# Kernel tuning notes

Measured on AMD Instinct MI355X. Metric: run time of the kernel, lower is better.

Reference implementation:

```python
import jax, jax.numpy as jnp
import numpy as np

BN_EPS = 1e-5

def conv1x1(x, w, b):
    # x: [B,C,H,W], w: [O,C], b: [O]
    return jnp.einsum('bchw,oc->bohw', x, w) + b[None, :, None, None]

def bn_inf(x, gamma, beta, mean, var):
    inv = gamma / jnp.sqrt(var + BN_EPS)
    return (x - mean[None, :, None, None]) * inv[None, :, None, None] + beta[None, :, None, None]

def setup_inputs() -> dict:
    key = jax.random.key(0)
    ks = jax.random.split(key, 24)
    B, Fg, Fl, Fi = 8, 256, 256, 64
    H = W = 64
    c8 = Fi // 8
    d = {}
    d['g'] = jax.random.normal(ks[0], (B, Fg, H, W), jnp.float32)
    d['x'] = jax.random.normal(ks[1], (B, Fl, H, W), jnp.float32)
    # W_g: conv1x1 + BN
    d['Wg_w'] = jax.random.normal(ks[2], (Fi, Fg), jnp.float32) * (1.0 / np.sqrt(Fg))
    d['Wg_b'] = jax.random.normal(ks[3], (Fi,), jnp.float32) * 0.02
    d['bng_gamma'] = jax.random.uniform(ks[4], (Fi,), jnp.float32, 0.5, 1.5)
    d['bng_beta'] = jax.random.normal(ks[5], (Fi,), jnp.float32) * 0.1
    d['bng_mean'] = jax.random.normal(ks[6], (Fi,), jnp.float32) * 0.1
    d['bng_var'] = jax.random.uniform(ks[7], (Fi,), jnp.float32, 0.5, 1.5)
    # W_x: conv1x1 + BN
    d['Wx_w'] = jax.random.normal(ks[8], (Fi, Fl), jnp.float32) * (1.0 / np.sqrt(Fl))
    d['Wx_b'] = jax.random.normal(ks[9], (Fi,), jnp.float32) * 0.02
    d['bnx_gamma'] = jax.random.uniform(ks[10], (Fi,), jnp.float32, 0.5, 1.5)
    d['bnx_beta'] = jax.random.normal(ks[11], (Fi,), jnp.float32) * 0.1
    d['bnx_mean'] = jax.random.normal(ks[12], (Fi,), jnp.float32) * 0.1
    d['bnx_var'] = jax.random.uniform(ks[13], (Fi,), jnp.float32, 0.5, 1.5)
    # psi: conv1x1 (Fi->1) + BN(1) + sigmoid
    d['psi_w'] = jax.random.normal(ks[14], (1, Fi), jnp.float32) * (1.0 / np.sqrt(Fi))
    d['psi_b'] = jax.random.normal(ks[15], (1,), jnp.float32) * 0.02
    d['bnp_gamma'] = jax.random.uniform(ks[16], (1,), jnp.float32, 0.5, 1.5)
    d['bnp_beta'] = jax.random.normal(ks[17], (1,), jnp.float32) * 0.1
    d['bnp_mean'] = jax.random.normal(ks[18], (1,), jnp.float32) * 0.1
    d['bnp_var'] = jax.random.uniform(ks[19], (1,), jnp.float32, 0.5, 1.5)
    # PAM convs
    d['pb_w'] = jax.random.normal(ks[20], (c8, Fi), jnp.float32) * (1.0 / np.sqrt(Fi))
    d['pb_b'] = jnp.zeros((c8,), jnp.float32)
    d['pc_w'] = jax.random.normal(ks[21], (c8, Fi), jnp.float32) * (1.0 / np.sqrt(Fi))
    d['pc_b'] = jnp.zeros((c8,), jnp.float32)
    d['pd_w'] = jax.random.normal(ks[22], (Fi, Fi), jnp.float32) * (1.0 / np.sqrt(Fi))
    d['pd_b'] = jnp.zeros((Fi,), jnp.float32)
    # scalar gates (torch inits to 0; use small nonzero to exercise the path)
    d['alpha'] = jax.random.normal(ks[23], (1,), jnp.float32) * 0.05
    d['cam_beta'] = jax.random.normal(jax.random.fold_in(key, 99), (1,), jnp.float32) * 0.05
    return d

def _cam(psi, cam_beta):
    B, C, H, W = psi.shape
    feat = psi.reshape(B, C, H * W)                       # [B,C,HW]
    att = jnp.einsum('bcn,bdn->bcd', feat, feat)          # [B,C,C]
    att_new = jnp.max(att, axis=-1, keepdims=True) - att  # max-subtract trick
    att = jax.nn.softmax(att_new, axis=-1)
    out = jnp.einsum('bcd,bdn->bcn', att, feat).reshape(B, C, H, W)
    return cam_beta[0] * out + psi

def _pam(psi, pb_w, pb_b, pc_w, pc_b, pd_w, pd_b, alpha):
    B, C, H, W = psi.shape
    HW = H * W
    fb = conv1x1(psi, pb_w, pb_b).reshape(B, -1, HW)      # [B,C/8,HW]
    fc = conv1x1(psi, pc_w, pc_b).reshape(B, -1, HW)      # [B,C/8,HW]
    energy = jnp.einsum('bki,bkj->bij', fb, fc)           # [B,HW,HW]
    att = jax.nn.softmax(energy, axis=-1)
    fd = conv1x1(psi, pd_w, pd_b).reshape(B, C, HW)       # [B,C,HW]
    out = jnp.einsum('bcj,bij->bci', fd, att).reshape(B, C, H, W)
    return alpha[0] * out + psi

def reference(g, x, Wg_w, Wg_b, bng_gamma, bng_beta, bng_mean, bng_var,
              Wx_w, Wx_b, bnx_gamma, bnx_beta, bnx_mean, bnx_var,
              psi_w, psi_b, bnp_gamma, bnp_beta, bnp_mean, bnp_var,
              pb_w, pb_b, pc_w, pc_b, pd_w, pd_b, alpha, cam_beta):
    g1 = bn_inf(conv1x1(g, Wg_w, Wg_b), bng_gamma, bng_beta, bng_mean, bng_var)
    x1 = bn_inf(conv1x1(x, Wx_w, Wx_b), bnx_gamma, bnx_beta, bnx_mean, bnx_var)
    psi = jax.nn.relu(g1 + x1)                            # [B,F_int,H,W]
    cam = _cam(psi, cam_beta)
    pam = _pam(psi, pb_w, pb_b, pc_w, pc_b, pd_w, pd_b, alpha)
    gate = bn_inf(conv1x1(cam * pam, psi_w, psi_b), bnp_gamma, bnp_beta, bnp_mean, bnp_var)
    da = jax.nn.sigmoid(gate)                             # [B,1,H,W]
    return x * da
```

## Files before the change

### kernel.cpp

```cpp
#include <hip/hip_runtime.h>
#include <hip/hip_bf16.h>
#include <math.h>

#define BB 8
#define CIN 256
#define FI 64
#define HW 4096
#define C8 8
#define EPS 1e-5f
#define LOG2E 1.4426950408889634f

typedef __attribute__((ext_vector_type(8))) short bf16x8;
typedef __attribute__((ext_vector_type(4))) float f32x4;
typedef __attribute__((ext_vector_type(4))) unsigned u32x4;
typedef unsigned short u16;

static __device__ __forceinline__ u16 f2b(float x) {
    unsigned u = __builtin_bit_cast(unsigned, x);
    return (u16)((u + 0x8000u) >> 16);
}
static __device__ __forceinline__ unsigned pk2(float a, float b) {
    unsigned ua = __builtin_bit_cast(unsigned, a);
    unsigned ub = __builtin_bit_cast(unsigned, b);
    return ((ua + 0x8000u) >> 16) | ((ub + 0x8000u) & 0xffff0000u);
}
static __device__ __forceinline__ unsigned cvtpk(float a, float b) {
    unsigned r;
    asm("v_cvt_pk_bf16_f32 %0, %1, %2" : "=v"(r) : "v"(a), "v"(b));
    return r;
}
static __device__ __forceinline__ float b2f(u16 v) {
    return __builtin_bit_cast(float, ((unsigned)v) << 16);
}

__global__ __launch_bounds__(256) void k_prep(
    const float* __restrict__ Wg, const float* __restrict__ Wgb,
    const float* __restrict__ gg, const float* __restrict__ gbeta,
    const float* __restrict__ gm, const float* __restrict__ gv,
    const float* __restrict__ Wx, const float* __restrict__ Wxb,
    const float* __restrict__ xg, const float* __restrict__ xbeta,
    const float* __restrict__ xm, const float* __restrict__ xv,
    const float* __restrict__ pbw, const float* __restrict__ pbb,
    const float* __restrict__ pcw, const float* __restrict__ pcb,
    const float* __restrict__ pdw, const float* __restrict__ pdb,
    u16* __restrict__ Wp, float* __restrict__ Cp,
    u16* __restrict__ Wcat, float* __restrict__ bcat)
{
    const int gid = blockIdx.x * 256 + threadIdx.x;
    for (int idx = gid; idx < FI * 512; idx += 4096) {
        int o = idx >> 9, k = idx & 511;
        float s, w;
        if (k < 256) { s = gg[o] * rsqrtf(gv[o] + EPS); w = Wg[o * 256 + k]; }
        else         { s = xg[o] * rsqrtf(xv[o] + EPS); w = Wx[o * 256 + k - 256]; }
        Wp[idx] = f2b(w * s);
    }
    for (int idx = gid; idx < 80 * 64; idx += 4096) {
        int row = idx >> 6, col = idx & 63;
        float w;
        if (row < 8)       w = pbw[row * 64 + col] * LOG2E;
        else if (row < 16) w = pcw[(row - 8) * 64 + col];
        else               w = pdw[(row - 16) * 64 + col];
        Wcat[idx] = f2b(w);
    }
    if (blockIdx.x == 0) {
        int tid = threadIdx.x;
        if (tid < FI) {
            float ig = gg[tid] * rsqrtf(gv[tid] + EPS);
            float ix = xg[tid] * rsqrtf(xv[tid] + EPS);
            Cp[tid] = (Wgb[tid] - gm[tid]) * ig + gbeta[tid]
                    + (Wxb[tid] - xm[tid]) * ix + xbeta[tid];
        }
        if (tid >= 64 && tid < 144) {
            int r = tid - 64;
            float bv = (r < 8) ? pbb[r] * LOG2E : (r < 16 ? pcb[r - 8] : pdb[r - 16]);
            bcat[r] = bv;
        }
    }
}

__global__ __launch_bounds__(256) void k_psi(
    const float* __restrict__ g, const float* __restrict__ x,
    const u16* __restrict__ Wp, const float* __restrict__ Cp,
    const u16* __restrict__ Wcat, const float* __restrict__ bcat,
    u16* __restrict__ psiB, u16* __restrict__ psiLo,
    u16* __restrict__ fbcT, u16* __restrict__ fdB)
{
    const int tid  = threadIdx.x;
    const int lane = tid & 63;
    const int w    = tid >> 6;
    const int n    = lane & 15;
    const int quad = lane >> 4;
    const int b    = blockIdx.y;
    const int p0   = blockIdx.x * 64;

    __shared__ u16 InT[64][72];
    __shared__ u16 Tbc[64][16];

    f32x4 acc[4];
#pragma unroll
    for (int mt = 0; mt < 4; ++mt) acc[mt] = (f32x4){0.f, 0.f, 0.f, 0.f};

    const size_t pxoff = (size_t)p0 + w * 16 + n;
#pragma unroll
    for (int kc = 0; kc < 8; ++kc) {
        const float* src = (kc < 4) ? g : x;
        const int ch0 = (kc & 3) * 64;
        const float* base = src + ((size_t)b * CIN + ch0 + quad * 8) * HW + pxoff;
#pragma unroll
        for (int ks = 0; ks < 2; ++ks) {
            const float* bp = base + (size_t)(ks * 32) * HW;
            float f0 = bp[0 * HW], f1 = bp[1 * HW], f2 = bp[2 * HW], f3 = bp[3 * HW];
            float f4 = bp[4 * HW], f5 = bp[5 * HW], f6 = bp[6 * HW], f7 = bp[7 * HW];
            u32x4 t = {pk2(f0, f1), pk2(f2, f3), pk2(f4, f5), pk2(f6, f7)};
            bf16x8 bfrag = __builtin_bit_cast(bf16x8, t);
            const int kglob = kc * 64 + ks * 32;
#pragma unroll
            for (int mt = 0; mt < 4; ++mt) {
                bf16x8 af = *(const bf16x8*)&Wp[(mt * 16 + n) * 512 + kglob + quad * 8];
                acc[mt] = __builtin_amdgcn_mfma_f32_16x16x32_bf16(
                              af, bfrag, acc[mt], 0, 0, 0);
            }
        }
    }

    float pv[4][4];
#pragma unroll
    for (int mt = 0; mt < 4; ++mt)
#pragma unroll
        for (int r = 0; r < 4; ++r) {
            int c = mt * 16 + quad * 4 + r;
            float v = acc[mt][r] + Cp[c];
            v = v > 0.f ? v : 0.f;
            pv[mt][r] = v;
            u16 hb = f2b(v);
            size_t idx = ((size_t)b * FI + c) * HW + p0 + w * 16 + n;
            psiB[idx]  = hb;
            psiLo[idx] = f2b(v - b2f(hb));
        }
#pragma unroll
    for (int mt = 0; mt < 4; ++mt) {
        *(unsigned*)&InT[w * 16 + n][mt * 16 + quad * 4]     = cvtpk(pv[mt][0], pv[mt][1]);
        *(unsigned*)&InT[w * 16 + n][mt * 16 + quad * 4 + 2] = cvtpk(pv[mt][2], pv[mt][3]);
    }
    __syncthreads();

    f32x4 facc[5];
#pragma unroll
    for (int nt = 0; nt < 5; ++nt) facc[nt] = (f32x4){0.f, 0.f, 0.f, 0.f};
#pragma unroll
    for (int ks = 0; ks < 2; ++ks) {
        bf16x8 af = *(const bf16x8*)&InT[w * 16 + n][ks * 32 + quad * 8];
#pragma unroll
        for (int nt = 0; nt < 5; ++nt) {
            bf16x8 bf = *(const bf16x8*)&Wcat[(nt * 16 + n) * FI + ks * 32 + quad * 8];
            facc[nt] = __builtin_amdgcn_mfma_f32_16x16x32_bf16(af, bf, facc[nt], 0, 0, 0);
        }
    }
    __syncthreads();

    {
        float bias = bcat[n];
#pragma unroll
        for (int r = 0; r < 4; ++r)
            Tbc[w * 16 + quad * 4 + r][n] = f2b(facc[0][r] + bias);
    }
#pragma unroll
    for (int nt = 1; nt < 5; ++nt) {
        int ch = (nt - 1) * 16 + n;
        float bias = bcat[nt * 16 + n];
        *(unsigned*)&InT[ch][w * 16 + quad * 4]     = cvtpk(facc[nt][0] + bias, facc[nt][1] + bias);
        *(unsigned*)&InT[ch][w * 16 + quad * 4 + 2] = cvtpk(facc[nt][2] + bias, facc[nt][3] + bias);
    }
    __syncthreads();
    {
        int row = tid >> 2, part = tid & 3;
        uint2 v = *(const uint2*)&Tbc[row][part * 4];
        *(uint2*)&fbcT[((size_t)b * HW + p0 + row) * 16 + part * 4] = v;
    }
#pragma unroll
    for (int rep = 0; rep < 2; ++rep) {
        int t = rep * 256 + tid;
        int ch = t >> 3, seg = t & 7;
        bf16x8 v = *(const bf16x8*)&InT[ch][seg * 8];
        *(bf16x8*)&fdB[((size_t)b * FI + ch) * HW + p0 + seg * 8] = v;
    }
}

__global__ __launch_bounds__(256) void k_gram(
    const u16* __restrict__ psiB, const u16* __restrict__ psiLo,
    float* __restrict__ Gp)
{
    const int tid  = threadIdx.x;
    const int lane = tid & 63;
    const int w    = tid >> 6;
    const int n    = lane & 15;
    const int quad = lane >> 4;
    const int s    = blockIdx.x;
    const int b    = blockIdx.y;
    const int zz   = blockIdx.z;

    f32x4 acc[2];
#pragma unroll
    for (int nt = 0; nt < 2; ++nt) acc[nt] = (f32x4){0.f, 0.f, 0.f, 0.f};

    for (int ks = 0; ks < 4; ++ks) {
        const int k0 = s * 128 + ks * 32;
        const size_t ra = ((size_t)b * FI + w * 16 + n) * HW + k0 + quad * 8;
        bf16x8 ah = *(const bf16x8*)&psiB[ra];
        bf16x8 al = *(const bf16x8*)&psiLo[ra];
#pragma unroll
        for (int nt = 0; nt < 2; ++nt) {
            const size_t rb = ((size_t)b * FI + zz * 32 + nt * 16 + n) * HW + k0 + quad * 8;
            bf16x8 bh = *(const bf16x8*)&psiB[rb];
            bf16x8 bl = *(const bf16x8*)&psiLo[rb];
            acc[nt] = __builtin_amdgcn_mfma_f32_16x16x32_bf16(ah, bh, acc[nt], 0, 0, 0);
            acc[nt] = __builtin_amdgcn_mfma_f32_16x16x32_bf16(ah, bl, acc[nt], 0, 0, 0);
            acc[nt] = __builtin_amdgcn_mfma_f32_16x16x32_bf16(al, bh, acc[nt], 0, 0, 0);
        }
    }
#pragma unroll
    for (int nt = 0; nt < 2; ++nt)
#pragma unroll
        for (int r = 0; r < 4; ++r) {
            int i = w * 16 + quad * 4 + r;
            Gp[(((size_t)s * 8 + b) * 64 + i) * 64 + zz * 32 + nt * 16 + n] = acc[nt][r];
        }
}

__global__ __launch_bounds__(256) void k_camsm(
    const float* __restrict__ Gp, float* __restrict__ att)
{
    const int tid = threadIdx.x, tx = tid & 63, ty = tid >> 6;
    const int b = blockIdx.x, i = blockIdx.y;
    __shared__ float part[4][64];

    float gs = 0.f;
#pragma unroll
    for (int j = 0; j < 8; ++j) {
        int s = ty * 8 + j;
        gs += Gp[(((size_t)s * 8 + b) * 64 + i) * 64 + tx];
    }
    part[ty][tx] = gs;
    __syncthreads();
    if (tid < 64) {
        float gsum = part[0][tx] + part[1][tx] + part[2][tx] + part[3][tx];
        float M = gsum;
#pragma unroll
        for (int msk = 1; msk < 64; msk <<= 1) M = fmaxf(M, __shfl_xor(M, msk));
        float a = M - gsum;
        float m2 = a;
#pragma unroll
        for (int msk = 1; msk < 64; msk <<= 1) m2 = fmaxf(m2, __shfl_xor(m2, msk));
        float p = __expf(a - m2);
        float ssum = p;
#pragma unroll
        for (int msk = 1; msk < 64; msk <<= 1) ssum += __shfl_xor(ssum, msk);
        att[((size_t)b * 64 + i) * 64 + tx] = p / ssum;
    }
}

__global__ __launch_bounds__(256) void k_pam(
    const u16* __restrict__ fbcT, const u16* __restrict__ fdB,
    u16* __restrict__ Opart, float* __restrict__ ml)
{
    const int tid  = threadIdx.x;
    const int lane = tid & 63;
    const int w    = tid >> 6;
    const int n    = lane & 15;
    const int quad = lane >> 4;
    const int b    = blockIdx.x;
    const int i0   = blockIdx.y * 64;
    const int p    = blockIdx.z;
    const int jstart = p * 32, jend = jstart + 32;

    __shared__ u16 Ks[2][68][8];
    __shared__ u16 Vs[2][64][64];
    __shared__ u16 Ps[4][16][64];

    if (tid < 16) {
        ((unsigned*)&Ks[0][64][0])[tid] = 0u;
        ((unsigned*)&Ks[1][64][0])[tid] = 0u;
    }

    bf16x8 qfrag = {};
    if (quad == 0)
        qfrag = *(const bf16x8*)&fbcT[((size_t)b * HW + i0 + w * 16 + n) * 16];

    const int kkey = tid >> 1, khalf = tid & 1;
    const int vch  = tid >> 3, vseg  = tid & 7;
    const int vslot = (vseg ^ (vch & 7)) << 3;
    const int pswz  = n & 7;

    const u16* kp = fbcT + ((size_t)b * HW + jstart * 64) * 16 + 8;
    const u16* vp = fdB + (size_t)b * FI * HW + jstart * 64;

    uint2 kr0 = make_uint2(0u, 0u), kr1 = make_uint2(0u, 0u);
    bf16x8 v0a, v0b, v1a, v1b;
    if (tid < 128) {
        kr0 = *(const uint2*)(kp + (size_t)kkey * 16 + khalf * 4);
        kr1 = *(const uint2*)(kp + 1024 + (size_t)kkey * 16 + khalf * 4);
    }
    v0a = *(const bf16x8*)(vp + (size_t)vch * HW + vseg * 8);
    v0b = *(const bf16x8*)(vp + (size_t)(32 + vch) * HW + vseg * 8);
    v1a = *(const bf16x8*)(vp + 64 + (size_t)vch * HW + vseg * 8);
    v1b = *(const bf16x8*)(vp + 64 + (size_t)(32 + vch) * HW + vseg * 8);

    f32x4 oacc[4];
#pragma unroll
    for (int mt = 0; mt < 4; ++mt) oacc[mt] = (f32x4){0.f, 0.f, 0.f, 0.f};
    float m = -1e30f, l = 0.f;

#define PAM_STEP(BUF)                                                           \
    {                                                                           \
        f32x4 s[4];                                                             \
        __builtin_amdgcn_s_setprio(1);                                          \
        _Pragma("unroll")                                                       \
        for (int mt = 0; mt < 4; ++mt) {                                        \
            bf16x8 af = *(const bf16x8*)&Ks[BUF][mt * 16 + n + quad][0];        \
            s[mt] = __builtin_amdgcn_mfma_f32_16x16x32_bf16(                    \
                        af, qfrag, (f32x4){0.f, 0.f, 0.f, 0.f}, 0, 0, 0);       \
        }                                                                       \
        __builtin_amdgcn_s_setprio(0);                                          \
        float cm = fmaxf(fmaxf(s[0][0], s[0][1]), s[0][2]);                     \
        cm = fmaxf(fmaxf(cm, s[0][3]), s[1][0]);                                \
        cm = fmaxf(fmaxf(cm, s[1][1]), s[1][2]);                                \
        cm = fmaxf(fmaxf(cm, s[1][3]), s[2][0]);                                \
        cm = fmaxf(fmaxf(cm, s[2][1]), s[2][2]);                                \
        cm = fmaxf(fmaxf(cm, s[2][3]), s[3][0]);                                \
        cm = fmaxf(fmaxf(cm, s[3][1]), s[3][2]);                                \
        cm = fmaxf(cm, s[3][3]);                                                \
        cm = fmaxf(cm, __shfl_xor(cm, 16));                                     \
        cm = fmaxf(cm, __shfl_xor(cm, 32));                                     \
        if (__any(cm > m + 8.f)) {                                              \
            float mnew  = fmaxf(m, cm);                                         \
            float scale = __builtin_amdgcn_exp2f(m - mnew);                     \
            l *= scale;                                                         \
            _Pragma("unroll")                                                   \
            for (int mt = 0; mt < 4; ++mt) {                                    \
                oacc[mt][0] *= scale; oacc[mt][1] *= scale;                     \
                oacc[mt][2] *= scale; oacc[mt][3] *= scale;                     \
            }                                                                   \
            m = mnew;                                                           \
        }                                                                       \
        float psum = 0.f;                                                       \
        unsigned pw[4][2];                                                      \
        _Pragma("unroll")                                                       \
        for (int mt = 0; mt < 4; ++mt) {                                        \
            float e0 = __builtin_amdgcn_exp2f(s[mt][0] - m);                    \
            float e1 = __builtin_amdgcn_exp2f(s[mt][1] - m);                    \
            float e2 = __builtin_amdgcn_exp2f(s[mt][2] - m);                    \
            float e3 = __builtin_amdgcn_exp2f(s[mt][3] - m);                    \
            psum += (e0 + e1) + (e2 + e3);                                      \
            pw[mt][0] = cvtpk(e0, e1);                                          \
            pw[mt][1] = cvtpk(e2, e3);                                          \
        }                                                                       \
        l += psum;                                                              \
        _Pragma("unroll")                                                       \
        for (int mt = 0; mt < 4; ++mt) {                                        \
            int so = (((mt * 2 + (quad >> 1)) ^ pswz) << 3) + ((quad & 1) << 2);\
            *(uint2*)&Ps[w][n][so] = make_uint2(pw[mt][0], pw[mt][1]);          \
        }                                                                       \
        __builtin_amdgcn_s_setprio(1);                                          \
        _Pragma("unroll")                                                       \
        for (int k0 = 0; k0 < 2; ++k0) {                                        \
            bf16x8 pf = *(const bf16x8*)&Ps[w][n][((k0 * 4 + quad) ^ pswz) << 3];\
            _Pragma("unroll")                                                   \
            for (int mt = 0; mt < 4; ++mt) {                                    \
                bf16x8 vf = *(const bf16x8*)                                    \
                    &Vs[BUF][mt * 16 + n][((k0 * 4 + quad) ^ pswz) << 3];       \
                oacc[mt] = __builtin_amdgcn_mfma_f32_16x16x32_bf16(             \
                               vf, pf, oacc[mt], 0, 0, 0);                      \
            }                                                                   \
        }                                                                       \
        __builtin_amdgcn_s_setprio(0);                                          \
    }

    for (int jc = jstart; jc < jend; jc += 2) {
        if (tid < 128) *(uint2*)&Ks[0][kkey][khalf * 4] = kr0;
        *(bf16x8*)&Vs[0][vch][vslot]      = v0a;
        *(bf16x8*)&Vs[0][32 + vch][vslot] = v0b;
        if (jc + 2 < jend) {
            if (tid < 128)
                kr0 = *(const uint2*)(kp + 2048 + (size_t)kkey * 16 + khalf * 4);
            v0a = *(const bf16x8*)(vp + 128 + (size_t)vch * HW + vseg * 8);
            v0b = *(const bf16x8*)(vp + 128 + (size_t)(32 + vch) * HW + vseg * 8);
        }
        __syncthreads();
        PAM_STEP(0)

        if (tid < 128) *(uint2*)&Ks[1][kkey][khalf * 4] = kr1;
        *(bf16x8*)&Vs[1][vch][vslot]      = v1a;
        *(bf16x8*)&Vs[1][32 + vch][vslot] = v1b;
        if (jc + 3 < jend) {
            if (tid < 128)
                kr1 = *(const uint2*)(kp + 3072 + (size_t)kkey * 16 + khalf * 4);
            v1a = *(const bf16x8*)(vp + 192 + (size_t)vch * HW + vseg * 8);
            v1b = *(const bf16x8*)(vp + 192 + (size_t)(32 + vch) * HW + vseg * 8);
        }
        kp += 2048;
        vp += 128;
        __syncthreads();
        PAM_STEP(1)
    }
#undef PAM_STEP

    l += __shfl_xor(l, 16);
    l += __shfl_xor(l, 32);
    const float rl = 1.f / l;
#pragma unroll
    for (int mt = 0; mt < 4; ++mt)
#pragma unroll
        for (int r = 0; r < 4; ++r) {
            int c = mt * 16 + quad * 4 + r;
            Opart[(((size_t)p * 8 + b) * FI + c) * HW + i0 + w * 16 + n] =
                f2b(oacc[mt][r] * rl);
        }
    if (quad == 0)
        ((float2*)ml)[((size_t)p * 8 + b) * HW + i0 + w * 16 + n] = make_float2(m, l);
}

__global__ __launch_bounds__(256) void k_final(
    const u16* __restrict__ psiB, const u16* __restrict__ psiLo,
    const float* __restrict__ att,
    const u16* __restrict__ Opart, const float* __restrict__ ml,
    const float* __restrict__ x,
    const float* __restrict__ psiw, const float* __restrict__ psib,
    const float* __restrict__ pg, const float* __restrict__ pbeta,
    const float* __restrict__ pm, const float* __restrict__ pv,
    const float* __restrict__ alpha, const float* __restrict__ camb,
    float* __restrict__ out)
{
    const int tid  = threadIdx.x;
    const int lane = tid & 63;
    const int w    = tid >> 6;
    const int n    = lane & 15;
    const int quad = lane >> 4;
    const int b = blockIdx.y, p0 = blockIdx.x * 64;

    __shared__ u16 Abf[64][64];
    __shared__ u16 tpB[64][64];
    __shared__ u16 tpLo[64][64];
    __shared__ float Wc0[64], Wc1[64], Pw[64], daL[64];
    __shared__ float Zp[4][64];

    {
        int c = tid >> 2, seg = tid & 3;
        const float* ap = &att[((size_t)b * 64 + c) * 64 + seg * 16];
        float4 v0 = *(const float4*)(ap);
        float4 v1 = *(const float4*)(ap + 4);
        float4 v2 = *(const float4*)(ap + 8);
        float4 v3 = *(const float4*)(ap + 12);
        float vv[16] = {v0.x, v0.y, v0.z, v0.w, v1.x, v1.y, v1.z, v1.w,
                        v2.x, v2.y, v2.z, v2.w, v3.x, v3.y, v3.z, v3.w};
#pragma unroll
        for (int j = 0; j < 8; ++j) {
            int d0 = seg * 16 + j * 2;
            int phys = (((d0 >> 3) ^ (c & 7)) << 3) | (d0 & 7);
            *(unsigned*)&Abf[c][phys] = cvtpk(vv[2 * j], vv[2 * j + 1]);
        }
    }
    {
        int px = tid & 63, grp = tid >> 6;
#pragma unroll
        for (int cc = 0; cc < 16; cc += 2) {
            int c = grp * 16 + cc;
            size_t i0 = ((size_t)b * FI + c) * HW + p0 + px;
            unsigned hb = ((unsigned)psiB[i0]) | (((unsigned)psiB[i0 + HW]) << 16);
            unsigned lb = ((unsigned)psiLo[i0]) | (((unsigned)psiLo[i0 + HW]) << 16);
            int phys = (((c >> 3) ^ (px & 7)) << 3) | (c & 7);
            *(unsigned*)&tpB[px][phys]  = hb;
            *(unsigned*)&tpLo[px][phys] = lb;
        }
    }
    if (tid < 64) {
        Pw[tid] = psiw[tid];
        float2 ml0 = ((const float2*)ml)[((size_t)0 * 8 + b) * HW + p0 + tid];
        float2 ml1 = ((const float2*)ml)[((size_t)1 * 8 + b) * HW + p0 + tid];
        float M  = fmaxf(ml0.x, ml1.x);
        float w0 = ml0.y * __builtin_amdgcn_exp2f(ml0.x - M);
        float w1 = ml1.y * __builtin_amdgcn_exp2f(ml1.x - M);
        float winv = 1.f / (w0 + w1);
        Wc0[tid] = w0 * winv; Wc1[tid] = w1 * winv;
    }
    __syncthreads();

    f32x4 acc[4];
#pragma unroll
    for (int nt = 0; nt < 4; ++nt) acc[nt] = (f32x4){0.f, 0.f, 0.f, 0.f};
#pragma unroll
    for (int ks = 0; ks < 2; ++ks) {
        int arow = w * 16 + n;
        bf16x8 af = *(const bf16x8*)&Abf[arow][((ks * 4 + quad) ^ (arow & 7)) << 3];
#pragma unroll
        for (int nt = 0; nt < 4; ++nt) {
            int brow = nt * 16 + n;
            int boff = ((ks * 4 + quad) ^ (brow & 7)) << 3;
            bf16x8 bh = *(const bf16x8*)&tpB[brow][boff];
            bf16x8 bl = *(const bf16x8*)&tpLo[brow][boff];
            acc[nt] = __builtin_amdgcn_mfma_f32_16x16x32_bf16(af, bh, acc[nt], 0, 0, 0);
            acc[nt] = __builtin_amdgcn_mfma_f32_16x16x32_bf16(af, bl, acc[nt], 0, 0, 0);
        }
    }

    const float al = alpha[0], cb = camb[0];
    float z[4] = {0.f, 0.f, 0.f, 0.f};
#pragma unroll
    for (int nt = 0; nt < 4; ++nt) {
        int px = nt * 16 + n;
        float w0 = Wc0[px], w1 = Wc1[px];
#pragma unroll
        for (int r = 0; r < 4; ++r) {
            int c = w * 16 + quad * 4 + r;
            int phys = (((c >> 3) ^ (px & 7)) << 3) | (c & 7);
            float ps  = b2f(tpB[px][phys]) + b2f(tpLo[px][phys]);
            float cam = cb * acc[nt][r] + ps;
            float oa = w0 * b2f(Opart[(((size_t)0 * 8 + b) * FI + c) * HW + p0 + px])
                     + w1 * b2f(Opart[(((size_t)1 * 8 + b) * FI + c) * HW + p0 + px]);
            float pam = al * oa + ps;
            z[nt] += Pw[c] * (cam * pam);
        }
    }
#pragma unroll
    for (int nt = 0; nt < 4; ++nt) {
        z[nt] += __shfl_xor(z[nt], 16);
        z[nt] += __shfl_xor(z[nt], 32);
    }
    if (quad == 0) {
#pragma unroll
        for (int nt = 0; nt < 4; ++nt) Zp[w][nt * 16 + n] = z[nt];
    }
    __syncthreads();
    if (tid < 64) {
        float zt = Zp[0][tid] + Zp[1][tid] + Zp[2][tid] + Zp[3][tid] + psib[0];
        float inv = pg[0] * rsqrtf(pv[0] + EPS);
        float gate = (zt - pm[0]) * inv + pbeta[0];
        daL[tid] = 1.f / (1.f + __expf(-gate));
    }
    __syncthreads();

    const int tx = lane;
    const float da = daL[tx];
#pragma unroll 8
    for (int r = 0; r < 64; ++r) {
        int cl = w + 4 * r;
        size_t idx = ((size_t)b * CIN + cl) * HW + p0 + tx;
        out[idx] = x[idx] * da;
    }
}

extern "C" void kernel_launch(void* const* d_in, const int* in_sizes, int n_in,
                              void* d_out, int out_size, void* d_ws, size_t ws_size,
                              hipStream_t stream)
{
    const float* g     = (const float*)d_in[0];
    const float* x     = (const float*)d_in[1];
    const float* Wg_w  = (const float*)d_in[2];
    const float* Wg_b  = (const float*)d_in[3];
    const float* bng_g = (const float*)d_in[4];
    const float* bng_b = (const float*)d_in[5];
    const float* bng_m = (const float*)d_in[6];
    const float* bng_v = (const float*)d_in[7];
    const float* Wx_w  = (const float*)d_in[8];
    const float* Wx_b  = (const float*)d_in[9];
    const float* bnx_g = (const float*)d_in[10];
    const float* bnx_b = (const float*)d_in[11];
    const float* bnx_m = (const float*)d_in[12];
    const float* bnx_v = (const float*)d_in[13];
    const float* psi_w = (const float*)d_in[14];
    const float* psi_b = (const float*)d_in[15];
    const float* bnp_g = (const float*)d_in[16];
    const float* bnp_b = (const float*)d_in[17];
    const float* bnp_m = (const float*)d_in[18];
    const float* bnp_v = (const float*)d_in[19];
    const float* pb_w  = (const float*)d_in[20];
    const float* pb_b  = (const float*)d_in[21];
    const float* pc_w  = (const float*)d_in[22];
    const float* pc_b  = (const float*)d_in[23];
    const float* pd_w  = (const float*)d_in[24];
    const float* pd_b  = (const float*)d_in[25];
    const float* alpha = (const float*)d_in[26];
    const float* camb  = (const float*)d_in[27];
    float* out = (float*)d_out;

    float* ws   = (float*)d_ws;
    u16*  psiB  = (u16*)(ws);
    u16*  psiLo = (u16*)(ws + 1048576);
    u16*  fbcT  = (u16*)(ws + 2097152);
    u16*  fdB   = (u16*)(ws + 2359296);
    float* att  = ws + 3407872;
    u16*  Wp    = (u16*)(ws + 3440640);
    float* Cp   = ws + 3457024;
    u16*  Wcat  = (u16*)(ws + 3457088);
    float* bcat = ws + 3459648;
    float* mlws = ws + 3459744;
    float* Gp   = ws + 3590816;
    u16*  Opart = (u16*)(ws + 3590816);

    k_prep<<<dim3(16), 256, 0, stream>>>(Wg_w, Wg_b, bng_g, bng_b, bng_m, bng_v,
                                         Wx_w, Wx_b, bnx_g, bnx_b, bnx_m, bnx_v,
                                         pb_w, pb_b, pc_w, pc_b, pd_w, pd_b,
                                         Wp, Cp, Wcat, bcat);
    k_psi<<<dim3(64, 8), 256, 0, stream>>>(g, x, Wp, Cp, Wcat, bcat,
                                           psiB, psiLo, fbcT, fdB);
    k_gram<<<dim3(32, 8, 2), 256, 0, stream>>>(psiB, psiLo, Gp);
    k_camsm<<<dim3(8, 64), 256, 0, stream>>>(Gp, att);
    k_pam<<<dim3(8, 64, 2), 256, 0, stream>>>(fbcT, fdB, Opart, mlws);
    k_final<<<dim3(64, 8), 256, 0, stream>>>(psiB, psiLo, att, Opart, mlws, x,
                                             psi_w, psi_b, bnp_g, bnp_b, bnp_m, bnp_v,
                                             alpha, camb, out);
}
```

Measured before the change: 244.7 us.

## Split PAM key range into four partitions and vectorize final gating store

Templates the PAM flash-attention kernel and the final combine kernel on the number of key partitions. When the workspace is large enough, it uses four partitions instead of two, doubling the grid to improve occupancy and combining more partial results in the final kernel. The final x*da loop also switches to float4 loads and stores. The cost is more partial-output traffic and merge work, plus a path that depends on workspace size.

```diff
diff --git a/kernel.cpp b/kernel.cpp
--- a/kernel.cpp
+++ b/kernel.cpp
@@ -259,6 +259,7 @@
     }
 }
 
+template<int P>
 __global__ __launch_bounds__(256) void k_pam(
     const u16* __restrict__ fbcT, const u16* __restrict__ fdB,
     u16* __restrict__ Opart, float* __restrict__ ml)
@@ -271,7 +272,8 @@
     const int b    = blockIdx.x;
     const int i0   = blockIdx.y * 64;
     const int p    = blockIdx.z;
-    const int jstart = p * 32, jend = jstart + 32;
+    constexpr int JPER = 64 / P;
+    const int jstart = p * JPER, jend = jstart + JPER;
 
     __shared__ u16 Ks[2][68][8];
     __shared__ u16 Vs[2][64][64];
@@ -419,6 +421,7 @@
         ((float2*)ml)[((size_t)p * 8 + b) * HW + i0 + w * 16 + n] = make_float2(m, l);
 }
 
+template<int P>
 __global__ __launch_bounds__(256) void k_final(
     const u16* __restrict__ psiB, const u16* __restrict__ psiLo,
     const float* __restrict__ att,
@@ -440,7 +443,9 @@
     __shared__ u16 Abf[64][64];
     __shared__ u16 tpB[64][64];
     __shared__ u16 tpLo[64][64];
-    __shared__ float Wc0[64], Wc1[64], Pw[64], daL[64];
+    __shared__ float WcA[P][64];
+    __shared__ float Pw[64];
+    __shared__ alignas(16) float daL[64];
     __shared__ float Zp[4][64];
 
     {
@@ -474,13 +479,22 @@
     }
     if (tid < 64) {
         Pw[tid] = psiw[tid];
-        float2 ml0 = ((const float2*)ml)[((size_t)0 * 8 + b) * HW + p0 + tid];
-        float2 ml1 = ((const float2*)ml)[((size_t)1 * 8 + b) * HW + p0 + tid];
-        float M  = fmaxf(ml0.x, ml1.x);
-        float w0 = ml0.y * __builtin_amdgcn_exp2f(ml0.x - M);
-        float w1 = ml1.y * __builtin_amdgcn_exp2f(ml1.x - M);
-        float winv = 1.f / (w0 + w1);
-        Wc0[tid] = w0 * winv; Wc1[tid] = w1 * winv;
+        float2 mlv[P];
+        float M = -1e30f;
+#pragma unroll
+        for (int pp = 0; pp < P; ++pp) {
+            mlv[pp] = ((const float2*)ml)[((size_t)pp * 8 + b) * HW + p0 + tid];
+            M = fmaxf(M, mlv[pp].x);
+        }
+        float wv[P], wsum = 0.f;
+#pragma unroll
+        for (int pp = 0; pp < P; ++pp) {
+            wv[pp] = mlv[pp].y * __builtin_amdgcn_exp2f(mlv[pp].x - M);
+            wsum += wv[pp];
+        }
+        float winv = 1.f / wsum;
+#pragma unroll
+        for (int pp = 0; pp < P; ++pp) WcA[pp][tid] = wv[pp] * winv;
     }
     __syncthreads();
 
@@ -507,15 +521,17 @@
 #pragma unroll
     for (int nt = 0; nt < 4; ++nt) {
         int px = nt * 16 + n;
-        float w0 = Wc0[px], w1 = Wc1[px];
 #pragma unroll
         for (int r = 0; r < 4; ++r) {
             int c = w * 16 + quad * 4 + r;
             int phys = (((c >> 3) ^ (px & 7)) << 3) | (c & 7);
             float ps  = b2f(tpB[px][phys]) + b2f(tpLo[px][phys]);
             float cam = cb * acc[nt][r] + ps;
-            float oa = w0 * b2f(Opart[(((size_t)0 * 8 + b) * FI + c) * HW + p0 + px])
-                     + w1 * b2f(Opart[(((size_t)1 * 8 + b) * FI + c) * HW + p0 + px]);
+            float oa = 0.f;
+#pragma unroll
+            for (int pp = 0; pp < P; ++pp)
+                oa += WcA[pp][px] *
+                      b2f(Opart[(((size_t)pp * 8 + b) * FI + c) * HW + p0 + px]);
             float pam = al * oa + ps;
             z[nt] += Pw[c] * (cam * pam);
         }
@@ -538,13 +554,17 @@
     }
     __syncthreads();
 
-    const int tx = lane;
-    const float da = daL[tx];
-#pragma unroll 8
-    for (int r = 0; r < 64; ++r) {
-        int cl = w + 4 * r;
-        size_t idx = ((size_t)b * CIN + cl) * HW + p0 + tx;
-        out[idx] = x[idx] * da;
+    {
+        const int pxg = tid & 15, chb = tid >> 4;
+        float4 daf = *(const float4*)&daL[pxg * 4];
+#pragma unroll
+        for (int r = 0; r < 16; ++r) {
+            int cl = chb + 16 * r;
+            size_t idx = ((size_t)b * CIN + cl) * HW + p0 + pxg * 4;
+            float4 xv = *(const float4*)&x[idx];
+            *(float4*)&out[idx] = make_float4(xv.x * daf.x, xv.y * daf.y,
+                                              xv.z * daf.z, xv.w * daf.w);
+        }
     }
 }
 
@@ -593,8 +613,10 @@
     u16*  Wcat  = (u16*)(ws + 3457088);
     float* bcat = ws + 3459648;
     float* mlws = ws + 3459744;
-    float* Gp   = ws + 3590816;
-    u16*  Opart = (u16*)(ws + 3590816);
+    float* Gp   = ws + 3721888;
+    u16*  Opart = (u16*)(ws + 3721888);
+
+    const bool p4 = ws_size >= (size_t)7916192 * 4;
 
     k_prep<<<dim3(16), 256, 0, stream>>>(Wg_w, Wg_b, bng_g, bng_b, bng_m, bng_v,
                                          Wx_w, Wx_b, bnx_g, bnx_b, bnx_m, bnx_v,
@@ -604,8 +626,15 @@
                                            psiB, psiLo, fbcT, fdB);
     k_gram<<<dim3(32, 8, 2), 256, 0, stream>>>(psiB, psiLo, Gp);
     k_camsm<<<dim3(8, 64), 256, 0, stream>>>(Gp, att);
-    k_pam<<<dim3(8, 64, 2), 256, 0, stream>>>(fbcT, fdB, Opart, mlws);
-    k_final<<<dim3(64, 8), 256, 0, stream>>>(psiB, psiLo, att, Opart, mlws, x,
-                                             psi_w, psi_b, bnp_g, bnp_b, bnp_m, bnp_v,
-                                             alpha, camb, out);
-}
+    if (p4) {
+        k_pam<4><<<dim3(8, 64, 4), 256, 0, stream>>>(fbcT, fdB, Opart, mlws);
+        k_final<4><<<dim3(64, 8), 256, 0, stream>>>(psiB, psiLo, att, Opart, mlws, x,
+                                                    psi_w, psi_b, bnp_g, bnp_b,
+                                                    bnp_m, bnp_v, alpha, camb, out);
+    } else {
+        k_pam<2><<<dim3(8, 64, 2), 256, 0, stream>>>(fbcT, fdB, Opart, mlws);
+        k_final<2><<<dim3(64, 8), 256, 0, stream>>>(psiB, psiLo, att, Opart, mlws, x,
+                                                    psi_w, psi_b, bnp_g, bnp_b,
+                                                    bnp_m, bnp_v, alpha, camb, out);
+    }
+}
```

After: 248.9 us. Within noise of the previous version (+1.7%).

## Merge gram and PAM kernels into one launch and vectorize final gating

Applied to the files above, without the earlier changes.

The Gram-matrix kernel and the PAM attention kernel become a single launch whose block index selects which body to run. This lets the two independent stages share the GPU concurrently and removes one launch. Because Gp and Opart previously aliased the same workspace, the fused path only runs when the workspace is large enough to move Opart to its own region. If it is too small, the old separate kernels run instead. The final x*da loop also switches to float4 loads and stores, with a new thread-to-pixel/channel mapping.

```diff
diff --git a/kernel.cpp b/kernel.cpp
--- a/kernel.cpp
+++ b/kernel.cpp
@@ -186,18 +186,15 @@
     }
 }
 
-__global__ __launch_bounds__(256) void k_gram(
+static __device__ __forceinline__ void gram_body(
+    int tid, int s, int b, int zz,
     const u16* __restrict__ psiB, const u16* __restrict__ psiLo,
     float* __restrict__ Gp)
 {
-    const int tid  = threadIdx.x;
     const int lane = tid & 63;
     const int w    = tid >> 6;
     const int n    = lane & 15;
     const int quad = lane >> 4;
-    const int s    = blockIdx.x;
-    const int b    = blockIdx.y;
-    const int zz   = blockIdx.z;
 
     f32x4 acc[2];
 #pragma unroll
@@ -227,59 +224,28 @@
         }
 }
 
-__global__ __launch_bounds__(256) void k_camsm(
-    const float* __restrict__ Gp, float* __restrict__ att)
-{
-    const int tid = threadIdx.x, tx = tid & 63, ty = tid >> 6;
-    const int b = blockIdx.x, i = blockIdx.y;
-    __shared__ float part[4][64];
-
-    float gs = 0.f;
-#pragma unroll
-    for (int j = 0; j < 8; ++j) {
-        int s = ty * 8 + j;
-        gs += Gp[(((size_t)s * 8 + b) * 64 + i) * 64 + tx];
-    }
-    part[ty][tx] = gs;
-    __syncthreads();
-    if (tid < 64) {
-        float gsum = part[0][tx] + part[1][tx] + part[2][tx] + part[3][tx];
-        float M = gsum;
-#pragma unroll
-        for (int msk = 1; msk < 64; msk <<= 1) M = fmaxf(M, __shfl_xor(M, msk));
-        float a = M - gsum;
-        float m2 = a;
-#pragma unroll
-        for (int msk = 1; msk < 64; msk <<= 1) m2 = fmaxf(m2, __shfl_xor(m2, msk));
-        float p = __expf(a - m2);
-        float ssum = p;
-#pragma unroll
-        for (int msk = 1; msk < 64; msk <<= 1) ssum += __shfl_xor(ssum, msk);
-        att[((size_t)b * 64 + i) * 64 + tx] = p / ssum;
-    }
-}
-
-__global__ __launch_bounds__(256) void k_pam(
+struct PamShared {
+    u16 Ks[2][68][8];
+    u16 Vs[2][64][64];
+    u16 Ps[4][16][64];
+};
+
+template<int P>
+static __device__ __forceinline__ void pam_body(
+    PamShared& sh, int tid, int b, int i0, int p,
     const u16* __restrict__ fbcT, const u16* __restrict__ fdB,
     u16* __restrict__ Opart, float* __restrict__ ml)
 {
-    const int tid  = threadIdx.x;
     const int lane = tid & 63;
     const int w    = tid >> 6;
     const int n    = lane & 15;
     const int quad = lane >> 4;
-    const int b    = blockIdx.x;
-    const int i0   = blockIdx.y * 64;
-    const int p    = blockIdx.z;
-    const int jstart = p * 32, jend = jstart + 32;
-
-    __shared__ u16 Ks[2][68][8];
-    __shared__ u16 Vs[2][64][64];
-    __shared__ u16 Ps[4][16][64];
+    constexpr int JPER = 64 / P;
+    const int jstart = p * JPER, jend = jstart + JPER;
 
     if (tid < 16) {
-        ((unsigned*)&Ks[0][64][0])[tid] = 0u;
-        ((unsigned*)&Ks[1][64][0])[tid] = 0u;
+        ((unsigned*)&sh.Ks[0][64][0])[tid] = 0u;
+        ((unsigned*)&sh.Ks[1][64][0])[tid] = 0u;
     }
 
     bf16x8 qfrag = {};
@@ -316,7 +282,7 @@
         __builtin_amdgcn_s_setprio(1);                                          \
         _Pragma("unroll")                                                       \
         for (int mt = 0; mt < 4; ++mt) {                                        \
-            bf16x8 af = *(const bf16x8*)&Ks[BUF][mt * 16 + n + quad][0];        \
+            bf16x8 af = *(const bf16x8*)&sh.Ks[BUF][mt * 16 + n + quad][0];     \
             s[mt] = __builtin_amdgcn_mfma_f32_16x16x32_bf16(                    \
                         af, qfrag, (f32x4){0.f, 0.f, 0.f, 0.f}, 0, 0, 0);       \
         }                                                                       \
@@ -358,16 +324,16 @@
         _Pragma("unroll")                                                       \
         for (int mt = 0; mt < 4; ++mt) {                                        \
             int so = (((mt * 2 + (quad >> 1)) ^ pswz) << 3) + ((quad & 1) << 2);\
-            *(uint2*)&Ps[w][n][so] = make_uint2(pw[mt][0], pw[mt][1]);          \
+            *(uint2*)&sh.Ps[w][n][so] = make_uint2(pw[mt][0], pw[mt][1]);       \
         }                                                                       \
         __builtin_amdgcn_s_setprio(1);                                          \
         _Pragma("unroll")                                                       \
         for (int k0 = 0; k0 < 2; ++k0) {                                        \
-            bf16x8 pf = *(const bf16x8*)&Ps[w][n][((k0 * 4 + quad) ^ pswz) << 3];\
+            bf16x8 pf = *(const bf16x8*)&sh.Ps[w][n][((k0 * 4 + quad) ^ pswz) << 3];\
             _Pragma("unroll")                                                   \
             for (int mt = 0; mt < 4; ++mt) {                                    \
                 bf16x8 vf = *(const bf16x8*)                                    \
-                    &Vs[BUF][mt * 16 + n][((k0 * 4 + quad) ^ pswz) << 3];       \
+                    &sh.Vs[BUF][mt * 16 + n][((k0 * 4 + quad) ^ pswz) << 3];    \
                 oacc[mt] = __builtin_amdgcn_mfma_f32_16x16x32_bf16(             \
                                vf, pf, oacc[mt], 0, 0, 0);                      \
             }                                                                   \
@@ -376,9 +342,9 @@
     }
 
     for (int jc = jstart; jc < jend; jc += 2) {
-        if (tid < 128) *(uint2*)&Ks[0][kkey][khalf * 4] = kr0;
-        *(bf16x8*)&Vs[0][vch][vslot]      = v0a;
-        *(bf16x8*)&Vs[0][32 + vch][vslot] = v0b;
+        if (tid < 128) *(uint2*)&sh.Ks[0][kkey][khalf * 4] = kr0;
+        *(bf16x8*)&sh.Vs[0][vch][vslot]      = v0a;
+        *(bf16x8*)&sh.Vs[0][32 + vch][vslot] = v0b;
         if (jc + 2 < jend) {
             if (tid < 128)
                 kr0 = *(const uint2*)(kp + 2048 + (size_t)kkey * 16 + khalf * 4);
@@ -388,9 +354,9 @@
         __syncthreads();
         PAM_STEP(0)
 
-        if (tid < 128) *(uint2*)&Ks[1][kkey][khalf * 4] = kr1;
-        *(bf16x8*)&Vs[1][vch][vslot]      = v1a;
-        *(bf16x8*)&Vs[1][32 + vch][vslot] = v1b;
+        if (tid < 128) *(uint2*)&sh.Ks[1][kkey][khalf * 4] = kr1;
+        *(bf16x8*)&sh.Vs[1][vch][vslot]      = v1a;
+        *(bf16x8*)&sh.Vs[1][32 + vch][vslot] = v1b;
         if (jc + 3 < jend) {
             if (tid < 128)
                 kr1 = *(const uint2*)(kp + 3072 + (size_t)kkey * 16 + khalf * 4);
@@ -417,6 +383,70 @@
         }
     if (quad == 0)
         ((float2*)ml)[((size_t)p * 8 + b) * HW + i0 + w * 16 + n] = make_float2(m, l);
+}
+
+__global__ __launch_bounds__(256) void k_pamgram(
+    const u16* __restrict__ fbcT, const u16* __restrict__ fdB,
+    const u16* __restrict__ psiB, const u16* __restrict__ psiLo,
+    u16* __restrict__ Opart, float* __restrict__ ml, float* __restrict__ Gp)
+{
+    __shared__ PamShared sh;
+    const int bid = blockIdx.x;
+    const int tid = threadIdx.x;
+    if (bid < 512) {
+        gram_body(tid, bid & 31, (bid >> 5) & 7, bid >> 8, psiB, psiLo, Gp);
+    } else {
+        const int pid = bid - 512;
+        pam_body<2>(sh, tid, pid & 7, ((pid >> 3) & 63) * 64, pid >> 9,
+                    fbcT, fdB, Opart, ml);
+    }
+}
+
+__global__ __launch_bounds__(256) void k_gram(
+    const u16* __restrict__ psiB, const u16* __restrict__ psiLo,
+    float* __restrict__ Gp)
+{
+    gram_body(threadIdx.x, blockIdx.x, blockIdx.y, blockIdx.z, psiB, psiLo, Gp);
+}
+__global__ __launch_bounds__(256) void k_pam(
+    const u16* __restrict__ fbcT, const u16* __restrict__ fdB,
+    u16* __restrict__ Opart, float* __restrict__ ml)
+{
+    __shared__ PamShared sh;
+    pam_body<2>(sh, threadIdx.x, blockIdx.x, blockIdx.y * 64, blockIdx.z,
+                fbcT, fdB, Opart, ml);
+}
+
+__global__ __launch_bounds__(256) void k_camsm(
+    const float* __restrict__ Gp, float* __restrict__ att)
+{
+    const int tid = threadIdx.x, tx = tid & 63, ty = tid >> 6;
+    const int b = blockIdx.x, i = blockIdx.y;
+    __shared__ float part[4][64];
+
+    float gs = 0.f;
+#pragma unroll
+    for (int j = 0; j < 8; ++j) {
+        int s = ty * 8 + j;
+        gs += Gp[(((size_t)s * 8 + b) * 64 + i) * 64 + tx];
+    }
+    part[ty][tx] = gs;
+    __syncthreads();
+    if (tid < 64) {
+        float gsum = part[0][tx] + part[1][tx] + part[2][tx] + part[3][tx];
+        float M = gsum;
+#pragma unroll
+        for (int msk = 1; msk < 64; msk <<= 1) M = fmaxf(M, __shfl_xor(M, msk));
+        float a = M - gsum;
+        float m2 = a;
+#pragma unroll
+        for (int msk = 1; msk < 64; msk <<= 1) m2 = fmaxf(m2, __shfl_xor(m2, msk));
+        float p = __expf(a - m2);
+        float ssum = p;
+#pragma unroll
+        for (int msk = 1; msk < 64; msk <<= 1) ssum += __shfl_xor(ssum, msk);
+        att[((size_t)b * 64 + i) * 64 + tx] = p / ssum;
+    }
 }
 
 __global__ __launch_bounds__(256) void k_final(
@@ -440,7 +470,8 @@
     __shared__ u16 Abf[64][64];
     __shared__ u16 tpB[64][64];
     __shared__ u16 tpLo[64][64];
-    __shared__ float Wc0[64], Wc1[64], Pw[64], daL[64];
+    __shared__ float Wc0[64], Wc1[64], Pw[64];
+    __shared__ alignas(16) float daL[64];
     __shared__ float Zp[4][64];
 
     {
@@ -538,13 +569,17 @@
     }
     __syncthreads();
 
-    const int tx = lane;
-    const float da = daL[tx];
-#pragma unroll 8
-    for (int r = 0; r < 64; ++r) {
-        int cl = w + 4 * r;
-        size_t idx = ((size_t)b * CIN + cl) * HW + p0 + tx;
-        out[idx] = x[idx] * da;
+    {
+        const int pxg = tid & 15, chb = tid >> 4;
+        float4 daf = *(const float4*)&daL[pxg * 4];
+#pragma unroll
+        for (int r = 0; r < 16; ++r) {
+            int cl = chb + 16 * r;
+            size_t idx = ((size_t)b * CIN + cl) * HW + p0 + pxg * 4;
+            float4 xv = *(const float4*)&x[idx];
+            *(float4*)&out[idx] = make_float4(xv.x * daf.x, xv.y * daf.y,
+                                              xv.z * daf.z, xv.w * daf.w);
+        }
     }
 }
 
@@ -594,7 +629,10 @@
     float* bcat = ws + 3459648;
     float* mlws = ws + 3459744;
     float* Gp   = ws + 3590816;
-    u16*  Opart = (u16*)(ws + 3590816);
+
+    const bool fused = ws_size >= (size_t)6736544 * 4;
+    u16* Opart = fused ? (u16*)(ws + 4639392)
+                       : (u16*)(ws + 3590816);
 
     k_prep<<<dim3(16), 256, 0, stream>>>(Wg_w, Wg_b, bng_g, bng_b, bng_m, bng_v,
                                          Wx_w, Wx_b, bnx_g, bnx_b, bnx_m, bnx_v,
@@ -602,9 +640,15 @@
                                          Wp, Cp, Wcat, bcat);
     k_psi<<<dim3(64, 8), 256, 0, stream>>>(g, x, Wp, Cp, Wcat, bcat,
                                            psiB, psiLo, fbcT, fdB);
-    k_gram<<<dim3(32, 8, 2), 256, 0, stream>>>(psiB, psiLo, Gp);
-    k_camsm<<<dim3(8, 64), 256, 0, stream>>>(Gp, att);
-    k_pam<<<dim3(8, 64, 2), 256, 0, stream>>>(fbcT, fdB, Opart, mlws);
+    if (fused) {
+        k_pamgram<<<dim3(1536), 256, 0, stream>>>(fbcT, fdB, psiB, psiLo,
+                                                  Opart, mlws, Gp);
+        k_camsm<<<dim3(8, 64), 256, 0, stream>>>(Gp, att);
+    } else {
+        k_gram<<<dim3(32, 8, 2), 256, 0, stream>>>(psiB, psiLo, Gp);
+        k_camsm<<<dim3(8, 64), 256, 0, stream>>>(Gp, att);
+        k_pam<<<dim3(8, 64, 2), 256, 0, stream>>>(fbcT, fdB, Opart, mlws);
+    }
     k_final<<<dim3(64, 8), 256, 0, stream>>>(psiB, psiLo, att, Opart, mlws, x,
                                              psi_w, psi_b, bnp_g, bnp_b, bnp_m, bnp_v,
                                              alpha, camb, out);
```

Result: no change. 245.6 us (+0.4%).
